# Kernel tuning notes

Measured on AMD Instinct MI355X. Metric: run time of the kernel, lower is better.

Reference implementation:

```python
import jax, jax.numpy as jnp
import numpy as np

EDGE_TYPES = 7  # hardcoded edgeNumAttr in the original module


def setup_inputs() -> dict:
    key = jax.random.key(0)
    ks = jax.random.split(key, 6)
    B, N, E, Fi, Fo = 2, 100000, 400000, 128, 128
    x = jax.random.normal(ks[0], (B, N, Fi), dtype=jnp.float32)
    # 7 per-edge-type Linear layers (weight stored as [in, out] for x @ W)
    W = jax.random.normal(ks[1], (EDGE_TYPES, Fi, Fo), dtype=jnp.float32) * 0.05
    b = jax.random.normal(ks[2], (EDGE_TYPES, Fo), dtype=jnp.float32) * 0.05
    adj_values = jax.random.normal(ks[3], (EDGE_TYPES, E), dtype=jnp.float32)
    end_nodes = jax.random.randint(ks[4], (EDGE_TYPES, E), 0, N, dtype=jnp.int32)
    start_nodes = jax.random.randint(ks[5], (EDGE_TYPES, E), 0, N, dtype=jnp.int32)
    return {"x": x, "W": W, "b": b, "adj_values": adj_values,
            "end_nodes": end_nodes, "start_nodes": start_nodes}


def reference(x, W, b, adj_values, end_nodes, start_nodes):
    # x: [B, N, Fi]; W: [7, Fi, Fo]; b: [7, Fo]
    # adj_values/end_nodes/start_nodes: [7, E]
    B, N, _ = x.shape
    Fo = W.shape[2]
    out = jnp.zeros((B, N, Fo), dtype=x.dtype)
    for i in range(EDGE_TYPES):  # fixed small structural loop, distinct weights
        h = jnp.einsum('bnf,fo->bno', x, W[i]) + b[i]          # dense projection [B,N,Fo]
        # batch_spmm #1: [E,N] sparse gather with edge weights -> per-edge messages
        msg = adj_values[i][None, :, None] * h[:, end_nodes[i], :]  # [B,E,Fo]
        # batch_spmm #2: [N,E] all-ones scatter-add back onto start nodes, accumulated
        out = out.at[:, start_nodes[i], :].add(msg)
    return out
```

## Files before the change

kernel.cpp:

```cpp
#include <hip/hip_runtime.h>
#include <hip/hip_bf16.h>

#define F 128
#define ET 7
#define NT 64
#define BSH 9
#define BW  (1 << BSH)
#define CHUNK 8192

typedef __attribute__((ext_vector_type(8))) short short8;
typedef __attribute__((ext_vector_type(4))) float f32x4;
typedef __attribute__((ext_vector_type(4))) unsigned uint4v;

static __device__ __forceinline__ unsigned f2bf(float f) {
    unsigned u = __builtin_bit_cast(unsigned, f);
    unsigned r = u + 0x7fffu + ((u >> 16) & 1u);
    return r >> 16;
}
static __device__ __forceinline__ float bf2f(unsigned short h) {
    unsigned u = ((unsigned)h) << 16;
    return __builtin_bit_cast(float, u);
}
static __device__ __forceinline__ float lo16(unsigned v) {
    return __builtin_bit_cast(float, v << 16);
}
static __device__ __forceinline__ float hi16(unsigned v) {
    return __builtin_bit_cast(float, v & 0xffff0000u);
}

__global__ __launch_bounds__(256) void prep_wfrag(const float* __restrict__ W,
                                                  unsigned short* __restrict__ Wfrag) {
    int tid = blockIdx.x * blockDim.x + threadIdx.x;
    if (tid >= ET * 2048) return;
    int i   = tid >> 11;
    int rem = tid & 2047;
    int c   = rem >> 8;
    int kk  = (rem >> 6) & 3;
    int l   = rem & 63;
    const float* Wi = W + (size_t)i * F * F;
    unsigned short* dst = Wfrag + (size_t)tid * 8;
    int o  = c * 16 + (l & 15);
    int kb = kk * 32 + 4 * (l >> 4);
#pragma unroll
    for (int e = 0; e < 8; ++e) {
        int k = kb + (e & 3) + 16 * (e >> 2);
        dst[e] = (unsigned short)f2bf(Wi[k * F + o]);
    }
}

__global__ __launch_bounds__(256) void xb_convert(const float* __restrict__ x,
                                                  unsigned* __restrict__ xb,
                                                  int N, long n_pairs) {
    long stride = (long)gridDim.x * blockDim.x;
    for (long t = (long)blockIdx.x * blockDim.x + threadIdx.x; t < n_pairs; t += stride) {
        long row = t >> 6;
        int  c   = (int)(t & 63);
        int  b   = row >= N;
        long n   = row - (long)b * N;
        float2 v = ((const float2*)x)[t];
        xb[(n << 7) + b * 64 + c] = f2bf(v.x) | (f2bf(v.y) << 16);
    }
}

__global__ __launch_bounds__(256) void hist_bins2(const int* __restrict__ startn,
                                                  int* __restrict__ bincnt,
                                                  int E, int nbins) {
    __shared__ int lcnt[BW];
    int i  = blockIdx.y;
    int e0 = blockIdx.x * CHUNK;
    int e1 = e0 + CHUNK < E ? e0 + CHUNK : E;
    int t  = threadIdx.x;
    for (int b = t; b < nbins; b += 256) lcnt[b] = 0;
    __syncthreads();
    for (int e = e0 + t; e < e1; e += 256)
        atomicAdd(&lcnt[startn[(size_t)i * E + e] >> BSH], 1);
    __syncthreads();
    for (int b = t; b < nbins; b += 256)
        if (lcnt[b]) atomicAdd(&bincnt[i * nbins + b], lcnt[b]);
}

__global__ __launch_bounds__(256) void scan_bins(const int* __restrict__ bincnt,
                                                 int* __restrict__ bases,
                                                 int* __restrict__ cursor,
                                                 int nbt, int totE,
                                                 int* __restrict__ offsets, int CN) {
    __shared__ int sh[256];
    int carry = 0;
    for (int base = 0; base < nbt; base += 256) {
        int idx = base + threadIdx.x;
        int v = idx < nbt ? bincnt[idx] : 0;
        __syncthreads();
        sh[threadIdx.x] = v;
        __syncthreads();
        for (int o = 1; o < 256; o <<= 1) {
            int t = (int)threadIdx.x >= o ? sh[threadIdx.x - o] : 0;
            __syncthreads();
            sh[threadIdx.x] += t;
            __syncthreads();
        }
        int incl = sh[threadIdx.x];
        int total = sh[255];
        if (idx < nbt) {
            int excl = incl - v + carry;
            bases[idx]  = excl;
            cursor[idx] = excl;
        }
        carry += total;
    }
    if (threadIdx.x == 0) {
        bases[nbt]   = totE;
        offsets[CN]  = totE;
    }
}

__global__ __launch_bounds__(256) void bucket_scatter2(const int* __restrict__ startn,
                                                       const int* __restrict__ endn,
                                                       const float* __restrict__ adj,
                                                       int* __restrict__ cursor,
                                                       int2* __restrict__ tmp,
                                                       int E, int nbins) {
    __shared__ int lcnt[BW];
    __shared__ int lbase[BW];
    int i  = blockIdx.y;
    int e0 = blockIdx.x * CHUNK;
    int e1 = e0 + CHUNK < E ? e0 + CHUNK : E;
    int t  = threadIdx.x;
    for (int b = t; b < nbins; b += 256) lcnt[b] = 0;
    __syncthreads();
    for (int e = e0 + t; e < e1; e += 256)
        atomicAdd(&lcnt[startn[(size_t)i * E + e] >> BSH], 1);
    __syncthreads();
    for (int b = t; b < nbins; b += 256) {
        int c = lcnt[b];
        lbase[b] = c ? atomicAdd(&cursor[i * nbins + b], c) : 0;
        lcnt[b] = 0;
    }
    __syncthreads();
    for (int e = e0 + t; e < e1; e += 256) {
        size_t g = (size_t)i * E + e;
        int sn = startn[g];
        int b  = sn >> BSH;
        int pos = lbase[b] + atomicAdd(&lcnt[b], 1);
        tmp[pos] = make_int2(endn[g] | ((sn & (BW - 1)) << 17),
                             __builtin_bit_cast(int, adj[g]));
    }
}

__global__ __launch_bounds__(256) void bin_sort(const int2* __restrict__ tmp,
                                                const int* __restrict__ bases,
                                                int* __restrict__ offsets,
                                                int2* __restrict__ payload,
                                                int N, int nbins) {
    __shared__ int cs[BW];
    __shared__ int ex[BW];
    __shared__ int sh[256];
    int i   = blockIdx.y;
    int b   = blockIdx.x;
    int bid = i * nbins + b;
    int base = bases[bid];
    int endp = bases[bid + 1];
    int b0   = b << BSH;
    int span = N - b0; if (span > BW) span = BW;
    int t = threadIdx.x;

    cs[t] = 0; cs[t + 256] = 0;
    __syncthreads();
    for (int k = base + t; k < endp; k += 256)
        atomicAdd(&cs[(tmp[k].x >> 17) & (BW - 1)], 1);
    __syncthreads();
    int c0 = cs[2 * t], c1 = cs[2 * t + 1];
    int ps = c0 + c1;
    sh[t] = ps;
    __syncthreads();
    for (int o = 1; o < 256; o <<= 1) {
        int v = t >= o ? sh[t - o] : 0;
        __syncthreads();
        sh[t] += v;
        __syncthreads();
    }
    int ep = sh[t] - ps;
    ex[2 * t] = ep;
    ex[2 * t + 1] = ep + c0;
    __syncthreads();
    if (t < span)       offsets[(size_t)i * N + b0 + t]       = base + ex[t];
    if (t + 256 < span) offsets[(size_t)i * N + b0 + t + 256] = base + ex[t + 256];
    cs[2 * t] = ex[2 * t];
    cs[2 * t + 1] = ex[2 * t + 1];
    __syncthreads();
    for (int k = base + t; k < endp; k += 256) {
        int2 p = tmp[k];
        int nib = (p.x >> 17) & (BW - 1);
        int pos = base + atomicAdd(&cs[nib], 1);
        payload[pos] = make_int2((p.x & 0x1FFFF) | ((nib & (NT - 1)) << 20), p.y);
    }
}

__global__ __launch_bounds__(256) void hist_kernel(const int* __restrict__ startn,
                                                   int* __restrict__ counts,
                                                   int N, int E, int totE) {
    int tid = blockIdx.x * 256 + threadIdx.x;
    if (tid >= totE) return;
    int i = tid / E;
    atomicAdd(&counts[i * N + startn[tid]], 1);
}

__global__ __launch_bounds__(256) void block_sum(const int* __restrict__ counts,
                                                 int* __restrict__ partials, int CN) {
    int gid = blockIdx.x * 256 + threadIdx.x;
    int v = gid < CN ? counts[gid] : 0;
#pragma unroll
    for (int off = 1; off < 64; off <<= 1) v += __shfl_xor(v, off);
    __shared__ int sh[4];
    if ((threadIdx.x & 63) == 0) sh[threadIdx.x >> 6] = v;
    __syncthreads();
    if (threadIdx.x == 0) partials[blockIdx.x] = sh[0] + sh[1] + sh[2] + sh[3];
}

__global__ __launch_bounds__(256) void scan_partials(int* __restrict__ partials, int nblk) {
    __shared__ int sh[256];
    int carry = 0;
    for (int base = 0; base < nblk; base += 256) {
        int idx = base + threadIdx.x;
        int v = idx < nblk ? partials[idx] : 0;
        __syncthreads();
        sh[threadIdx.x] = v;
        __syncthreads();
        for (int o = 1; o < 256; o <<= 1) {
            int t = (int)threadIdx.x >= o ? sh[threadIdx.x - o] : 0;
            __syncthreads();
            sh[threadIdx.x] += t;
            __syncthreads();
        }
        int incl = sh[threadIdx.x];
        int total = sh[255];
        if (idx < nblk) partials[idx] = incl - v + carry;
        carry += total;
    }
}

__global__ __launch_bounds__(256) void scan_blocks(const int* __restrict__ counts,
                                                   const int* __restrict__ partials,
                                                   int* __restrict__ offsets,
                                                   int* __restrict__ cursor,
                                                   int CN, int totE) {
    __shared__ int sh[256];
    int gid = blockIdx.x * 256 + threadIdx.x;
    int v = gid < CN ? counts[gid] : 0;
    sh[threadIdx.x] = v;
    __syncthreads();
    for (int o = 1; o < 256; o <<= 1) {
        int t = (int)threadIdx.x >= o ? sh[threadIdx.x - o] : 0;
        __syncthreads();
        sh[threadIdx.x] += t;
        __syncthreads();
    }
    int excl = sh[threadIdx.x] - v + partials[blockIdx.x];
    if (gid < CN) { offsets[gid] = excl; cursor[gid] = excl; }
    if (gid == CN - 1) offsets[CN] = totE;
}

__global__ __launch_bounds__(256) void fill_csr(const int* __restrict__ startn,
                                                const int* __restrict__ endn,
                                                const float* __restrict__ adj,
                                                int* __restrict__ cursor,
                                                int2* __restrict__ payload,
                                                int N, int E, int totE) {
    int tid = blockIdx.x * 256 + threadIdx.x;
    if (tid >= totE) return;
    int i = tid / E;
    int sn = startn[tid];
    int pos = atomicAdd(&cursor[i * N + sn], 1);
    int px = endn[tid] | ((sn & (NT - 1)) << 20);
    payload[pos] = make_int2(px, __builtin_bit_cast(int, adj[tid]));
}

__global__ __launch_bounds__(512, 4) void fused_agg_gemm(
        const unsigned* __restrict__ xb,
        const unsigned short* __restrict__ Wfrag,
        const float* __restrict__ bias,
        const int* __restrict__ offsets,
        const int2* __restrict__ payload,
        float* __restrict__ out, int N) {
    __shared__ unsigned ylds[128 * 64];
    __shared__ float sadjl[ET][NT];
    __shared__ int offs[ET][NT + 1];

    int tid  = threadIdx.x;
    int wave = tid >> 6;
    int lane = tid & 63;
    int hl   = lane & 31;
    int hb   = lane >> 5;
    int lr   = lane & 15;
    int lg   = lane >> 4;
    int n0   = blockIdx.x * NT;

    if (tid < ET * (NT + 1)) {
        int i = tid / (NT + 1);
        int j = tid - i * (NT + 1);
        int n = n0 + j;
        ((int*)offs)[tid] = offsets[i * N + (n < N ? n : N)];
    }

    f32x4 acc[8];
#pragma unroll
    for (int c = 0; c < 8; ++c) acc[c] = (f32x4){0.f, 0.f, 0.f, 0.f};

    __syncthreads();

    const unsigned laneoff = (hb << 6) + (hl << 1);
    const int colw = hl << 1;

    for (int i = 0; i < ET; ++i) {
        int base = offs[i][0];
        int tot  = offs[i][NT] - base;
        int tgt_s = base + (int)(((long)tot * wave) >> 3);
        int tgt_e = base + (int)(((long)tot * (wave + 1)) >> 3);
        int oj = offs[i][lane];
        unsigned long long ms = __ballot(oj >= tgt_s);
        unsigned long long me = __ballot(oj >= tgt_e);
        int js = ms ? (__ffsll(ms) - 1) : NT;
        int je = (wave == 7) ? NT : (me ? (__ffsll(me) - 1) : NT);
        int kb = offs[i][js];
        int ke = offs[i][je];

        int cur = -1;
        float a0 = 0.f, a1 = 0.f, a2 = 0.f, a3 = 0.f, asum = 0.f;
        for (int k = kb; k < ke; k += 8) {
            int2 p[8];
            uint2 v[8];
#pragma unroll
            for (int j = 0; j < 8; ++j) {
                int idx = (k + j < ke) ? k + j : ke - 1;
                p[j] = payload[idx];
            }
#pragma unroll
            for (int j = 0; j < 8; ++j) {
                unsigned o32 = ((unsigned)(p[j].x & 0xFFFFF) << 7) | laneoff;
                v[j] = *(const uint2*)(xb + o32);
            }
#pragma unroll
            for (int j = 0; j < 8; ++j) {
                bool ok = (k + j) < ke;
                float w = ok ? __builtin_bit_cast(float, p[j].y) : 0.f;
                int nl = (p[j].x >> 20) & (NT - 1);
                if (ok && nl != cur) {
                    if (cur >= 0) {
                        unsigned pk0 = f2bf(a0) | (f2bf(a1) << 16);
                        unsigned pk1 = f2bf(a2) | (f2bf(a3) << 16);
                        int r = hb * NT + cur;
                        *(uint2*)&ylds[(r * 64 + colw) ^ ((r & 7) << 2)] = make_uint2(pk0, pk1);
                        if (lane == 0) sadjl[i][cur] = asum;
                    }
                    cur = nl;
                    a0 = a1 = a2 = a3 = asum = 0.f;
                }
                asum += w;
                a0 += w * lo16(v[j].x); a1 += w * hi16(v[j].x);
                a2 += w * lo16(v[j].y); a3 += w * hi16(v[j].y);
            }
        }
        if (cur >= 0) {
            unsigned pk0 = f2bf(a0) | (f2bf(a1) << 16);
            unsigned pk1 = f2bf(a2) | (f2bf(a3) << 16);
            int r = hb * NT + cur;
            *(uint2*)&ylds[(r * 64 + colw) ^ ((r & 7) << 2)] = make_uint2(pk0, pk1);
            if (lane == 0) sadjl[i][cur] = asum;
        }
        for (int j = js; j < je; ++j) {
            if (offs[i][j + 1] == offs[i][j]) {
                int r = hb * NT + j;
                *(uint2*)&ylds[(r * 64 + colw) ^ ((r & 7) << 2)] = make_uint2(0u, 0u);
                if (lane == 0) sadjl[i][j] = 0.f;
            }
        }
        __syncthreads();

        int row = wave * 16 + lr;
        int s = (row & 7) << 2;
#pragma unroll
        for (int kk = 0; kk < 4; ++kk) {
            int d0 = (row * 64 + kk * 16 + lg * 2) ^ s;
            int d1 = (row * 64 + kk * 16 + lg * 2 + 8) ^ s;
            uint2 c0 = *(const uint2*)&ylds[d0];
            uint2 c1 = *(const uint2*)&ylds[d1];
            uint4v av = {c0.x, c0.y, c1.x, c1.y};
            short8 afrag = __builtin_bit_cast(short8, av);
            const unsigned short* wbp = Wfrag + ((size_t)i * 2048 + (size_t)kk * 64 + lane) * 8;
#pragma unroll
            for (int c = 0; c < 8; ++c) {
                short8 bfrag = *(const short8*)(wbp + (size_t)c * 2048);
                acc[c] = __builtin_amdgcn_mfma_f32_16x16x32_bf16(afrag, bfrag, acc[c], 0, 0, 0);
            }
        }
        __syncthreads();
    }

#pragma unroll
    for (int c = 0; c < 8; ++c) {
        int col = c * 16 + lr;
        float bv[ET];
#pragma unroll
        for (int i = 0; i < ET; ++i) bv[i] = bias[i * F + col];
#pragma unroll
        for (int j = 0; j < 4; ++j) {
            int row = wave * 16 + lg * 4 + j;
            int nl = row & (NT - 1);
            int b  = row >> 6;
            int n  = n0 + nl;
            float vv = acc[c][j];
#pragma unroll
            for (int i = 0; i < ET; ++i) vv += sadjl[i][nl] * bv[i];
            if (n < N) out[((size_t)(b * N + n)) * F + col] = vv;
        }
    }
}

__global__ __launch_bounds__(256) void gemm_h(const float* __restrict__ x,
                                              const unsigned short* __restrict__ Wfrag,
                                              const float* __restrict__ bias,
                                              unsigned short* __restrict__ hb,
                                              int M) {
    int wave = threadIdx.x >> 6;
    int lane = threadIdx.x & 63;
    int row_base = blockIdx.x * 128 + wave * 32;
    int lr = lane & 15;
    int lg = lane >> 4;
    f32x4 acc[2][8];
#pragma unroll
    for (int t = 0; t < 2; ++t)
#pragma unroll
        for (int c = 0; c < 8; ++c)
            acc[t][c] = (f32x4){0.f, 0.f, 0.f, 0.f};
#pragma unroll
    for (int kk = 0; kk < 4; ++kk) {
        int k0 = kk * 32 + 4 * lg;
        short8 afrag[2];
#pragma unroll
        for (int t = 0; t < 2; ++t) {
            int r = row_base + t * 16 + lr;
            r = r < M ? r : M - 1;
            float4 v0 = *(const float4*)(x + (size_t)r * F + k0);
            float4 v1 = *(const float4*)(x + (size_t)r * F + k0 + 16);
            short8 a;
            a[0] = (short)f2bf(v0.x); a[1] = (short)f2bf(v0.y);
            a[2] = (short)f2bf(v0.z); a[3] = (short)f2bf(v0.w);
            a[4] = (short)f2bf(v1.x); a[5] = (short)f2bf(v1.y);
            a[6] = (short)f2bf(v1.z); a[7] = (short)f2bf(v1.w);
            afrag[t] = a;
        }
#pragma unroll
        for (int c = 0; c < 8; ++c) {
            short8 bfrag = *(const short8*)(Wfrag + (size_t)((c * 4 + kk) * 64 + lane) * 8);
            acc[0][c] = __builtin_amdgcn_mfma_f32_16x16x32_bf16(afrag[0], bfrag, acc[0][c], 0, 0, 0);
            acc[1][c] = __builtin_amdgcn_mfma_f32_16x16x32_bf16(afrag[1], bfrag, acc[1][c], 0, 0, 0);
        }
    }
#pragma unroll
    for (int c = 0; c < 8; ++c) {
        int o = c * 16 + lr;
        float bvv = bias[o];
#pragma unroll
        for (int t = 0; t < 2; ++t)
#pragma unroll
            for (int j = 0; j < 4; ++j) {
                int r = row_base + t * 16 + lg * 4 + j;
                if (r < M) hb[(size_t)r * F + o] = (unsigned short)f2bf(acc[t][c][j] + bvv);
            }
    }
}

__global__ __launch_bounds__(256) void edge_scatter(const unsigned short* __restrict__ hb,
                                                    const float* __restrict__ adj,
                                                    const int* __restrict__ endn,
                                                    const int* __restrict__ startn,
                                                    float* __restrict__ out,
                                                    int N, int E) {
    int e = blockIdx.x;
    if (e >= E) return;
    int b = threadIdx.x >> 7;
    int f = threadIdx.x & 127;
    float a = adj[e];
    int en = endn[e];
    int sn = startn[e];
    float v = a * bf2f(hb[((size_t)(b * N + en)) * F + f]);
    unsafeAtomicAdd(&out[((size_t)(b * N + sn)) * F + f], v);
}

__global__ __launch_bounds__(256) void edge_fused_slow(const float* __restrict__ x,
                                                       const float* __restrict__ W,
                                                       const float* __restrict__ bias,
                                                       const float* __restrict__ adj,
                                                       const int* __restrict__ endn,
                                                       const int* __restrict__ startn,
                                                       float* __restrict__ out,
                                                       int N, int E) {
    __shared__ float xrow[2][F];
    int e = blockIdx.x;
    if (e >= E) return;
    int b = threadIdx.x >> 7;
    int f = threadIdx.x & 127;
    int en = endn[e], sn = startn[e];
    xrow[b][f] = x[((size_t)(b * N + en)) * F + f];
    __syncthreads();
    float acc = bias[f];
#pragma unroll 8
    for (int k = 0; k < F; ++k) acc += xrow[b][k] * W[k * F + f];
    unsafeAtomicAdd(&out[((size_t)(b * N + sn)) * F + f], adj[e] * acc);
}

extern "C" void kernel_launch(void* const* d_in, const int* in_sizes, int n_in,
                              void* d_out, int out_size, void* d_ws, size_t ws_size,
                              hipStream_t stream) {
    const float* x      = (const float*)d_in[0];
    const float* W      = (const float*)d_in[1];
    const float* bias   = (const float*)d_in[2];
    const float* adj    = (const float*)d_in[3];
    const int*   endn   = (const int*)d_in[4];
    const int*   startn = (const int*)d_in[5];

    const int B = 2;
    const int N = in_sizes[0] / (B * F);
    const int E = in_sizes[3] / ET;
    const int M = B * N;
    const int totE = ET * E;
    const int CN = ET * N;
    const int nblk = (CN + 255) / 256;
    const int nbins = (N + BW - 1) >> BSH;
    const int nbt = ET * nbins;
    float* out = (float*)d_out;

    size_t off = 0;
    auto take = [&](size_t bytes) { size_t o = off; off = (off + bytes + 255) & ~(size_t)255; return o; };
    size_t o_wfrag   = take((size_t)ET * F * F * 2);
    size_t o_bincnt  = take((size_t)nbt * 4);
    size_t o_bases   = take((size_t)(nbt + 1) * 4);
    size_t o_bcur    = take((size_t)nbt * 4);
    size_t o_offsets = take((size_t)(CN + 1) * 4);
    size_t o_tmp     = take((size_t)totE * 8);
    size_t o_payload = take((size_t)totE * 8);
    size_t o_xb      = take((size_t)M * F * 2);
    size_t need_bucket = off;

    off = 0;
    size_t q_wfrag    = take((size_t)ET * F * F * 2);
    size_t q_counts   = take((size_t)CN * 4);
    size_t q_offsets  = take((size_t)(CN + 1) * 4);
    size_t q_cursor   = take((size_t)CN * 4);
    size_t q_partials = take((size_t)nblk * 4);
    size_t q_payload  = take((size_t)totE * 8);
    size_t q_xb       = take((size_t)M * F * 2);
    size_t need_old_csr = off;
    size_t need_r1 = 256 * 1024 + (size_t)M * F * 2;

    char* ws = (char*)d_ws;

    if (ws_size >= need_bucket && N < (1 << 17)) {
        unsigned short* Wfrag = (unsigned short*)(ws + o_wfrag);
        int*  bincnt  = (int*)(ws + o_bincnt);
        int*  bases   = (int*)(ws + o_bases);
        int*  bcur    = (int*)(ws + o_bcur);
        int*  offsets = (int*)(ws + o_offsets);
        int2* tmp     = (int2*)(ws + o_tmp);
        int2* payload = (int2*)(ws + o_payload);
        unsigned* xbuf = (unsigned*)(ws + o_xb);

        hipMemsetAsync(bincnt, 0, (size_t)nbt * 4, stream);
        prep_wfrag<<<(ET * 2048 + 255) / 256, 256, 0, stream>>>(W, Wfrag);
        xb_convert<<<2048, 256, 0, stream>>>(x, xbuf, N, (long)M * (F / 2));
        dim3 cg((E + CHUNK - 1) / CHUNK, ET);
        hist_bins2<<<cg, 256, 0, stream>>>(startn, bincnt, E, nbins);
        scan_bins<<<1, 256, 0, stream>>>(bincnt, bases, bcur, nbt, totE, offsets, CN);
        bucket_scatter2<<<cg, 256, 0, stream>>>(startn, endn, adj, bcur, tmp, E, nbins);
        dim3 bg(nbins, ET);
        bin_sort<<<bg, 256, 0, stream>>>(tmp, bases, offsets, payload, N, nbins);

        int fgrid = (N + NT - 1) / NT;
        fused_agg_gemm<<<fgrid, 512, 0, stream>>>(xbuf, Wfrag, bias, offsets, payload, out, N);
    } else if (ws_size >= need_old_csr) {
        unsigned short* Wfrag = (unsigned short*)(ws + q_wfrag);
        int*  counts   = (int*)(ws + q_counts);
        int*  offsets  = (int*)(ws + q_offsets);
        int*  cursor   = (int*)(ws + q_cursor);
        int*  partials = (int*)(ws + q_partials);
        int2* payload  = (int2*)(ws + q_payload);
        unsigned* xbuf = (unsigned*)(ws + q_xb);

        hipMemsetAsync(counts, 0, (size_t)CN * 4, stream);
        prep_wfrag<<<(ET * 2048 + 255) / 256, 256, 0, stream>>>(W, Wfrag);
        xb_convert<<<2048, 256, 0, stream>>>(x, xbuf, N, (long)M * (F / 2));
        hist_kernel<<<(totE + 255) / 256, 256, 0, stream>>>(startn, counts, N, E, totE);
        block_sum<<<nblk, 256, 0, stream>>>(counts, partials, CN);
        scan_partials<<<1, 256, 0, stream>>>(partials, nblk);
        scan_blocks<<<nblk, 256, 0, stream>>>(counts, partials, offsets, cursor, CN, totE);
        fill_csr<<<(totE + 255) / 256, 256, 0, stream>>>(startn, endn, adj, cursor, payload, N, E, totE);

        int fgrid = (N + NT - 1) / NT;
        fused_agg_gemm<<<fgrid, 512, 0, stream>>>(xbuf, Wfrag, bias, offsets, payload, out, N);
    } else if (ws_size >= need_r1) {
        hipMemsetAsync(out, 0, (size_t)out_size * sizeof(float), stream);
        unsigned short* Wfrag = (unsigned short*)d_ws;
        unsigned short* hbuf  = (unsigned short*)((char*)d_ws + 256 * 1024);
        prep_wfrag<<<(ET * 2048 + 255) / 256, 256, 0, stream>>>(W, Wfrag);
        int ggrid = (M + 127) / 128;
        for (int i = 0; i < ET; ++i) {
            gemm_h<<<ggrid, 256, 0, stream>>>(x, Wfrag + (size_t)i * F * F, bias + i * F, hbuf, M);
            edge_scatter<<<E, 256, 0, stream>>>(hbuf, adj + (size_t)i * E, endn + (size_t)i * E,
                                                startn + (size_t)i * E, out, N, E);
        }
    } else {
        hipMemsetAsync(out, 0, (size_t)out_size * sizeof(float), stream);
        for (int i = 0; i < ET; ++i) {
            edge_fused_slow<<<E, 256, 0, stream>>>(x, W + (size_t)i * F * F, bias + i * F,
                                                   adj + (size_t)i * E, endn + (size_t)i * E,
                                                   startn + (size_t)i * E, out, N, E);
        }
    }
}
```

Measured before the change: 504.4 us.

## Split edge gather into two passes by source-node half for cache locality

Each block now walks its edge list twice, gathering only source nodes in the lower half of the node range on the first pass and the upper half on the second. The goal is to shrink the working set of x rows touched at once so more gathers hit in cache. In exchange the payload is read twice, the LDS tile is zero-initialised up front, partial sums go through a read-modify-write in bf16 (extra rounding), and the per-lane gathers are now serial and conditional instead of batched eight at a time.

```diff
diff --git a/kernel.cpp b/kernel.cpp
--- a/kernel.cpp
+++ b/kernel.cpp
@@ -293,6 +293,7 @@
     int lr   = lane & 15;
     int lg   = lane >> 4;
     int n0   = blockIdx.x * NT;
+    int half0 = N >> 1;
 
     if (tid < ET * (NT + 1)) {
         int i = tid / (NT + 1);
@@ -311,6 +312,10 @@
     const int colw = hl << 1;
 
     for (int i = 0; i < ET; ++i) {
+#pragma unroll
+        for (int u = 0; u < 16; ++u) ylds[tid + u * 512] = 0u;
+        if (tid < NT) sadjl[i][tid] = 0.f;
+
         int base = offs[i][0];
         int tot  = offs[i][NT] - base;
         int tgt_s = base + (int)(((long)tot * wave) >> 3);
@@ -323,64 +328,68 @@
         int kb = offs[i][js];
         int ke = offs[i][je];
 
-        int cur = -1;
-        float a0 = 0.f, a1 = 0.f, a2 = 0.f, a3 = 0.f, asum = 0.f;
-        for (int k = kb; k < ke; k += 8) {
-            int2 p[8];
-            uint2 v[8];
-#pragma unroll
-            for (int j = 0; j < 8; ++j) {
-                int idx = (k + j < ke) ? k + j : ke - 1;
-                p[j] = payload[idx];
+        __syncthreads();
+
+        for (int s = 0; s < 2; ++s) {
+            int cur = -1;
+            float a0 = 0.f, a1 = 0.f, a2 = 0.f, a3 = 0.f, asum = 0.f;
+            for (int k = kb; k < ke; k += 8) {
+                int2 p[8];
+#pragma unroll
+                for (int j = 0; j < 8; ++j) {
+                    int idx = (k + j < ke) ? k + j : ke - 1;
+                    p[j] = payload[idx];
+                }
+#pragma unroll
+                for (int j = 0; j < 8; ++j) {
+                    bool ok = (k + j) < ke;
+                    int en = p[j].x & 0xFFFFF;
+                    bool in = ok && ((en < half0) == (s == 0));
+                    if (in) {
+                        float w = __builtin_bit_cast(float, p[j].y);
+                        int nl = (p[j].x >> 20) & (NT - 1);
+                        if (nl != cur) {
+                            if (cur >= 0) {
+                                int r = hb * NT + cur;
+                                unsigned ad = (unsigned)((r * 64 + colw) ^ ((r & 7) << 2));
+                                uint2 oldv = *(uint2*)&ylds[ad];
+                                float o0 = lo16(oldv.x) + a0, o1 = hi16(oldv.x) + a1;
+                                float o2 = lo16(oldv.y) + a2, o3 = hi16(oldv.y) + a3;
+                                *(uint2*)&ylds[ad] =
+                                    make_uint2(f2bf(o0) | (f2bf(o1) << 16),
+                                               f2bf(o2) | (f2bf(o3) << 16));
+                                if (lane == 0) sadjl[i][cur] += asum;
+                            }
+                            cur = nl;
+                            a0 = a1 = a2 = a3 = asum = 0.f;
+                        }
+                        unsigned o32 = ((unsigned)en << 7) | laneoff;
+                        uint2 v = *(const uint2*)(xb + o32);
+                        asum += w;
+                        a0 += w * lo16(v.x); a1 += w * hi16(v.x);
+                        a2 += w * lo16(v.y); a3 += w * hi16(v.y);
+                    }
+                }
             }
-#pragma unroll
-            for (int j = 0; j < 8; ++j) {
-                unsigned o32 = ((unsigned)(p[j].x & 0xFFFFF) << 7) | laneoff;
-                v[j] = *(const uint2*)(xb + o32);
+            if (cur >= 0) {
+                int r = hb * NT + cur;
+                unsigned ad = (unsigned)((r * 64 + colw) ^ ((r & 7) << 2));
+                uint2 oldv = *(uint2*)&ylds[ad];
+                float o0 = lo16(oldv.x) + a0, o1 = hi16(oldv.x) + a1;
+                float o2 = lo16(oldv.y) + a2, o3 = hi16(oldv.y) + a3;
+                *(uint2*)&ylds[ad] = make_uint2(f2bf(o0) | (f2bf(o1) << 16),
+                                                f2bf(o2) | (f2bf(o3) << 16));
+                if (lane == 0) sadjl[i][cur] += asum;
             }
-#pragma unroll
-            for (int j = 0; j < 8; ++j) {
-                bool ok = (k + j) < ke;
-                float w = ok ? __builtin_bit_cast(float, p[j].y) : 0.f;
-                int nl = (p[j].x >> 20) & (NT - 1);
-                if (ok && nl != cur) {
-                    if (cur >= 0) {
-                        unsigned pk0 = f2bf(a0) | (f2bf(a1) << 16);
-                        unsigned pk1 = f2bf(a2) | (f2bf(a3) << 16);
-                        int r = hb * NT + cur;
-                        *(uint2*)&ylds[(r * 64 + colw) ^ ((r & 7) << 2)] = make_uint2(pk0, pk1);
-                        if (lane == 0) sadjl[i][cur] = asum;
-                    }
-                    cur = nl;
-                    a0 = a1 = a2 = a3 = asum = 0.f;
-                }
-                asum += w;
-                a0 += w * lo16(v[j].x); a1 += w * hi16(v[j].x);
-                a2 += w * lo16(v[j].y); a3 += w * hi16(v[j].y);
-            }
-        }
-        if (cur >= 0) {
-            unsigned pk0 = f2bf(a0) | (f2bf(a1) << 16);
-            unsigned pk1 = f2bf(a2) | (f2bf(a3) << 16);
-            int r = hb * NT + cur;
-            *(uint2*)&ylds[(r * 64 + colw) ^ ((r & 7) << 2)] = make_uint2(pk0, pk1);
-            if (lane == 0) sadjl[i][cur] = asum;
-        }
-        for (int j = js; j < je; ++j) {
-            if (offs[i][j + 1] == offs[i][j]) {
-                int r = hb * NT + j;
-                *(uint2*)&ylds[(r * 64 + colw) ^ ((r & 7) << 2)] = make_uint2(0u, 0u);
-                if (lane == 0) sadjl[i][j] = 0.f;
-            }
-        }
-        __syncthreads();
+            __syncthreads();
+        }
 
         int row = wave * 16 + lr;
-        int s = (row & 7) << 2;
+        int s2 = (row & 7) << 2;
 #pragma unroll
         for (int kk = 0; kk < 4; ++kk) {
-            int d0 = (row * 64 + kk * 16 + lg * 2) ^ s;
-            int d1 = (row * 64 + kk * 16 + lg * 2 + 8) ^ s;
+            int d0 = (row * 64 + kk * 16 + lg * 2) ^ s2;
+            int d1 = (row * 64 + kk * 16 + lg * 2 + 8) ^ s2;
             uint2 c0 = *(const uint2*)&ylds[d0];
             uint2 c1 = *(const uint2*)&ylds[d1];
             uint4v av = {c0.x, c0.y, c1.x, c1.y};
```

Result: slower. 850.9 us (+68.7%).
